# Optimization experiments

Hardware: AMD Instinct MI355X
Metric: run time of the kernel (lower is better)

The kernel has to match this reference:

```python
import jax, jax.numpy as jnp
import numpy as np
import math

B, S, F, H, E = 2, 1024, 512, 2048, 8
EPS = 1e-10

def setup_inputs() -> dict:
    key = jax.random.key(0)
    ks = jax.random.split(key, 6)
    s1 = math.sqrt(1.0 / (F + H))  # complex_xavier_init std for F->H
    s2 = math.sqrt(1.0 / (H + F))  # std for H->F
    return {
        'x_r': jax.random.normal(ks[0], (B, S, F), jnp.float32),
        'x_i': jax.random.normal(ks[1], (B, S, F), jnp.float32),
        'Wr1': jax.random.normal(ks[2], (E, F, H), jnp.float32) * s1,
        'Wi1': jax.random.normal(ks[3], (E, F, H), jnp.float32) * s1,
        'br1': jnp.zeros((E, H), jnp.float32),
        'bi1': jnp.zeros((E, H), jnp.float32),
        'mb': jnp.zeros((E, H), jnp.float32),  # ModReLU bias
        'Wr2': jax.random.normal(ks[4], (E, H, F), jnp.float32) * s2,
        'Wi2': jax.random.normal(ks[5], (E, H, F), jnp.float32) * s2,
        'br2': jnp.zeros((E, F), jnp.float32),
        'bi2': jnp.zeros((E, F), jnp.float32),
    }

def reference(x_r, x_i, Wr1, Wi1, br1, bi1, mb, Wr2, Wi2, br2, bi2):
    n_exp = Wr1.shape[0]
    # --- PhaseRouter: deterministic top-1 routing by mean token phase ---
    phase = jnp.arctan2(x_i, x_r)                      # angle(x), (B,S,F)
    mean_cos = jnp.mean(jnp.cos(phase), axis=-1)
    mean_sin = jnp.mean(jnp.sin(phase), axis=-1)
    token_phase = jnp.arctan2(mean_sin, mean_cos)      # (B,S)
    norm_phase = (token_phase + jnp.pi) / (2 * jnp.pi)
    idx = jnp.clip(jnp.floor(norm_phase * n_exp).astype(jnp.int32), 0, n_exp - 1)
    probs = jax.nn.one_hot(idx, n_exp, dtype=x_r.dtype)  # (B,S,E)
    # --- dense all-expert complex MLP (as in source: every expert on every token) ---
    # layer 1: complex linear F->H, per expert
    h_r = (jnp.einsum('bsf,efh->ebsh', x_r, Wr1) - jnp.einsum('bsf,efh->ebsh', x_i, Wi1)
           + br1[:, None, None, :])
    h_i = (jnp.einsum('bsf,efh->ebsh', x_r, Wi1) + jnp.einsum('bsf,efh->ebsh', x_i, Wr1)
           + bi1[:, None, None, :])
    # ModReLU: relu(|z|+b) * z/(|z|+eps)
    amp = jnp.sqrt(h_r * h_r + h_i * h_i + EPS)
    scale = jax.nn.relu(amp + mb[:, None, None, :]) / (amp + EPS)
    h_r = scale * h_r
    h_i = scale * h_i
    # layer 2: complex linear H->F, per expert
    y_r = (jnp.einsum('ebsh,ehf->ebsf', h_r, Wr2) - jnp.einsum('ebsh,ehf->ebsf', h_i, Wi2)
           + br2[:, None, None, :])
    y_i = (jnp.einsum('ebsh,ehf->ebsf', h_r, Wi2) + jnp.einsum('ebsh,ehf->ebsf', h_i, Wr2)
           + bi2[:, None, None, :])
    # combine: expert_weight * mask == probs * probs (one-hot, 0/1)
    w = probs * probs                                   # (B,S,E)
    out_r = jnp.einsum('ebsf,bse->bsf', y_r, w)
    out_i = jnp.einsum('ebsf,bse->bsf', y_i, w)
    return jnp.stack([out_r, out_i])                    # (2,B,S,F): real, imag
```

## Files before the change

kernel.cpp:

```cpp
#include <hip/hip_runtime.h>
#include <hip/hip_bf16.h>

#define TOKENS 2048
#define FDIM 512
#define HDIM 2048
#define NEXP 8
#define PI_F 3.14159265358979323846f

typedef __attribute__((ext_vector_type(8))) short bf16x8;
typedef __attribute__((ext_vector_type(4))) float f32x4;

__device__ __forceinline__ unsigned short f2bf(float f) {
  unsigned int u = __float_as_uint(f);
  unsigned int r = (u + 0x7fffu + ((u >> 16) & 1u)) >> 16;
  return (unsigned short)r;
}

__device__ __forceinline__ void gload16(const void* g, void* l) {
  __builtin_amdgcn_global_load_lds(
      (const __attribute__((address_space(1))) unsigned int*)g,
      (__attribute__((address_space(3))) unsigned int*)l, 16, 0, 0);
}

template<int K, int N>
__device__ __forceinline__ void pack_w_body64(
    const float* __restrict__ Wr, const float* __restrict__ Wi,
    short* __restrict__ Wp, int b, float (*tr)[33], float (*ti)[33])
{
  constexpr int NT_ = N / 32;
  int per_e = (K / 64) * NT_;
  int e = b / per_e;
  int rem = b % per_e;
  int k0 = (rem / NT_) * 64, n0 = (rem % NT_) * 32;
  int tid = threadIdx.x;
  int row = tid >> 2, c8 = (tid & 3) * 8;
  const float* wr = Wr + ((size_t)e * K + k0 + row) * N + n0 + c8;
  const float* wi = Wi + ((size_t)e * K + k0 + row) * N + n0 + c8;
  float4 a0 = *(const float4*)(wr);
  float4 a1 = *(const float4*)(wr + 4);
  float4 b0 = *(const float4*)(wi);
  float4 b1 = *(const float4*)(wi + 4);
  *(float4*)&tr[row][c8] = a0;  *(float4*)&tr[row][c8 + 4] = a1;
  *(float4*)&ti[row][c8] = b0;  *(float4*)&ti[row][c8 + 4] = b1;
  __syncthreads();
  int nl = tid >> 3, k8 = (tid & 7) * 8;
  unsigned short pr[8], pi[8];
  #pragma unroll
  for (int j = 0; j < 8; ++j) {
    pr[j] = f2bf(tr[k8 + j][nl]);
    pi[j] = f2bf(ti[k8 + j][nl]);
  }
  size_t d0 = (((size_t)e * 2 + 0) * N + n0 + nl) * K + k0 + k8;
  size_t d1 = (((size_t)e * 2 + 1) * N + n0 + nl) * K + k0 + k8;
  *(int4*)(Wp + d0) = *(const int4*)pr;
  *(int4*)(Wp + d1) = *(const int4*)pi;
}

template<int K, int N>
__device__ __forceinline__ void pack_w2x(
    const float* __restrict__ Wr, const float* __restrict__ Wi,
    short* __restrict__ Wp, int b, float (*tr)[33], float (*ti)[33])
{
  constexpr int NT_ = N / 32;
  int per_e = (K / 128) * NT_;
  int e = b / per_e;
  int rem = b % per_e;
  int k0 = (rem / NT_) * 128, n0 = (rem % NT_) * 32;
  int tid = threadIdx.x;
  int row = tid >> 2, c8 = (tid & 3) * 8;
  const float* wr = Wr + ((size_t)e * K + k0 + row) * N + n0 + c8;
  const float* wi = Wi + ((size_t)e * K + k0 + row) * N + n0 + c8;
  const float* wr1 = wr + (size_t)64 * N;
  const float* wi1 = wi + (size_t)64 * N;
  float4 a00 = *(const float4*)(wr);
  float4 a01 = *(const float4*)(wr + 4);
  float4 b00 = *(const float4*)(wi);
  float4 b01 = *(const float4*)(wi + 4);
  float4 a10 = *(const float4*)(wr1);
  float4 a11 = *(const float4*)(wr1 + 4);
  float4 b10 = *(const float4*)(wi1);
  float4 b11 = *(const float4*)(wi1 + 4);
  int nl = tid >> 3, k8 = (tid & 7) * 8;
  size_t d0 = (((size_t)e * 2 + 0) * N + n0 + nl) * K + k0 + k8;
  size_t d1 = (((size_t)e * 2 + 1) * N + n0 + nl) * K + k0 + k8;
  *(float4*)&tr[row][c8] = a00;  *(float4*)&tr[row][c8 + 4] = a01;
  *(float4*)&ti[row][c8] = b00;  *(float4*)&ti[row][c8 + 4] = b01;
  __syncthreads();
  {
    unsigned short pr[8], pi[8];
    #pragma unroll
    for (int j = 0; j < 8; ++j) {
      pr[j] = f2bf(tr[k8 + j][nl]);
      pi[j] = f2bf(ti[k8 + j][nl]);
    }
    *(int4*)(Wp + d0) = *(const int4*)pr;
    *(int4*)(Wp + d1) = *(const int4*)pi;
  }
  __syncthreads();
  *(float4*)&tr[row][c8] = a10;  *(float4*)&tr[row][c8 + 4] = a11;
  *(float4*)&ti[row][c8] = b10;  *(float4*)&ti[row][c8 + 4] = b11;
  __syncthreads();
  {
    unsigned short pr[8], pi[8];
    #pragma unroll
    for (int j = 0; j < 8; ++j) {
      pr[j] = f2bf(tr[k8 + j][nl]);
      pi[j] = f2bf(ti[k8 + j][nl]);
    }
    *(int4*)(Wp + d0 + 64) = *(const int4*)pr;
    *(int4*)(Wp + d1 + 64) = *(const int4*)pi;
  }
}

__global__ __launch_bounds__(256, 2) void route_packx_w1_kernel(
    const float* __restrict__ xr, const float* __restrict__ xi,
    int* __restrict__ idx,
    short* __restrict__ Ar, short* __restrict__ Ai,
    const float* __restrict__ Wr1, const float* __restrict__ Wi1,
    short* __restrict__ W1p)
{
  __shared__ float tr[64][33], ti[64][33];
  int bid = blockIdx.x;
  if (bid < 256) {
    int tid = threadIdx.x;
    int t = bid * 8 + (tid >> 5);
    int l = tid & 31;
    const float* r  = xr + (size_t)t * FDIM;
    const float* im = xi + (size_t)t * FDIM;
    float sc = 0.f, ss = 0.f;
    #pragma unroll
    for (int p = 0; p < 4; ++p) {
      int f = p * 128 + l * 4;
      float4 a4 = *(const float4*)(r + f);
      float4 b4 = *(const float4*)(im + f);
      float av[4] = {a4.x, a4.y, a4.z, a4.w};
      float bv[4] = {b4.x, b4.y, b4.z, b4.w};
      #pragma unroll
      for (int j = 0; j < 4; ++j) {
        float h2 = av[j] * av[j] + bv[j] * bv[j];
        if (h2 > 0.f) {
          float rs = rsqrtf(h2);
          sc += av[j] * rs;
          ss += bv[j] * rs;
        } else {
          sc += 1.f;
        }
      }
    }
    #pragma unroll
    for (int off = 16; off > 0; off >>= 1) {
      sc += __shfl_down(sc, off, 32);
      ss += __shfl_down(ss, off, 32);
    }
    if (l == 0) {
      float phase = atan2f(ss, sc);
      float norm = (phase + PI_F) / (2.f * PI_F);
      int e = (int)floorf(norm * (float)NEXP);
      e = min(max(e, 0), NEXP - 1);
      idx[t] = e;
    }
  } else if (bid < 256 + 1024) {
    int gid = (bid - 256) * 256 + threadIdx.x;
    int i = gid >> 7;
    int c4 = (gid & 127) * 4;
    float4 r = *(const float4*)(xr + (size_t)i * FDIM + c4);
    float4 m = *(const float4*)(xi + (size_t)i * FDIM + c4);
    unsigned short orr[4] = { f2bf(r.x), f2bf(r.y), f2bf(r.z), f2bf(r.w) };
    unsigned short oii[4] = { f2bf(m.x), f2bf(m.y), f2bf(m.z), f2bf(m.w) };
    *(int2*)(Ar + (size_t)i * FDIM + c4) = *(const int2*)orr;
    *(int2*)(Ai + (size_t)i * FDIM + c4) = *(const int2*)oii;
  } else {
    pack_w2x<FDIM, HDIM>(Wr1, Wi1, W1p, bid - 1280, tr, ti);
  }
}

__global__ __launch_bounds__(256) void scatter_kernel(
    const int* __restrict__ idx, int* __restrict__ counts,
    int* __restrict__ offs, int* __restrict__ perm, int* __restrict__ rexp)
{
  __shared__ int base_e[NEXP];
  __shared__ int totals[NEXP];
  __shared__ int tcnt[256][NEXP];
  int tid = threadIdx.x;
  int t0 = tid * 8;
  int eo[8];
  int loc[NEXP];
  #pragma unroll
  for (int e = 0; e < NEXP; ++e) loc[e] = 0;
  #pragma unroll
  for (int j = 0; j < 8; ++j) { eo[j] = idx[t0 + j]; loc[eo[j]]++; }
  #pragma unroll
  for (int e = 0; e < NEXP; ++e) tcnt[tid][e] = loc[e];
  __syncthreads();
  if (tid < NEXP) {
    int e = tid, run = 0;
    for (int i = 0; i < 256; ++i) { int v = tcnt[i][e]; tcnt[i][e] = run; run += v; }
    totals[e] = run;
    counts[e] = run;
  }
  __syncthreads();
  if (tid == 0) {
    int acc = 0;
    for (int e = 0; e < NEXP; ++e) { base_e[e] = acc; offs[e] = acc; acc += totals[e]; }
  }
  __syncthreads();
  #pragma unroll
  for (int e = 0; e < NEXP; ++e) loc[e] = base_e[e] + tcnt[tid][e];
  #pragma unroll
  for (int j = 0; j < 8; ++j) {
    int e = eo[j];
    int pos = loc[e]++;
    perm[pos] = t0 + j;
    rexp[pos] = e;
  }
}

template<int LDK, int NC, int NX, int NSPLIT, bool IS_L1>
__device__ __forceinline__ void gemm_body(
    int gbid, int xcd, short* AsB, short* WsB,
    const short* __restrict__ Apr, const short* __restrict__ Api,
    const short* __restrict__ Wp,
    const int* __restrict__ counts, const int* __restrict__ offs,
    const int* __restrict__ perm,
    const float* __restrict__ bre, const float* __restrict__ bim,
    const float* __restrict__ mb,
    short* __restrict__ Or, short* __restrict__ Oi,
    unsigned int* __restrict__ P)
{
  constexpr int PBE = NX * 8 * NSPLIT;
  constexpr int KCH = LDK / NSPLIT;
  constexpr int KT = KCH / 32;
  int virt = xcd * PBE + (gbid >> 3);
  int e = virt / PBE, rem = virt % PBE;
  int x = rem % NX;
  int q = rem / NX;
  int y = q & 7, s = q >> 3;
  int cnt = counts[e];
  int row0 = y * 64;
  if (row0 >= cnt) return;
  int base = offs[e];
  int n0c = x * 64;
  int kbase = s * KCH;

  int tid = threadIdx.x;
  int lane = tid & 63;
  int w = tid >> 6, wm = w >> 1, wn = w & 1;
  int lr = lane & 15, g = lane >> 4;
  int ssw = g ^ ((lr >> 1) & 3);

  int srl = tid >> 2, slt = tid & 3;
  int sc = (slt ^ ((srl >> 1) & 3)) * 16;
  int arow = min(row0 + srl, cnt - 1);
  size_t asrc;
  if constexpr (IS_L1) asrc = (size_t)perm[base + arow] * LDK + kbase;
  else                 asrc = (size_t)(base + arow) * LDK + kbase;
  const char* pAr = (const char*)(Apr + asrc) + sc;
  const char* pAi = (const char*)(Api + asrc) + sc;
  const short* We = Wp + (size_t)e * 2 * NC * LDK;
  const char* pW0 = (const char*)(We + (size_t)(n0c + srl) * LDK + kbase) + sc;
  const char* pW1 = (const char*)(We + ((size_t)NC + n0c + srl) * LDK + kbase) + sc;

  auto STAGE = [&](int buf, int t) {
    char* ab = (char*)AsB + buf * 8192;
    gload16(pAr + t * 64, ab + tid * 16);
    gload16(pAi + t * 64, ab + 4096 + tid * 16);
    char* wb = (char*)WsB + buf * 8192;
    gload16(pW0 + t * 64, wb + tid * 16);
    gload16(pW1 + t * 64, wb + 4096 + tid * 16);
  };

  f32x4 accr[2][2], acci[2][2];
  #pragma unroll
  for (int m = 0; m < 2; ++m)
    #pragma unroll
    for (int n = 0; n < 2; ++n) { accr[m][n] = 0.f; acci[m][n] = 0.f; }

  const bf16x8 SGN = {(short)0x8000, (short)0x8000, (short)0x8000, (short)0x8000,
                      (short)0x8000, (short)0x8000, (short)0x8000, (short)0x8000};

  auto COMPUTE = [&](int buf) {
    const short* Ab = AsB + buf * 4096;
    const short* Wb = WsB + buf * 4096;
    bf16x8 ar[2], ai[2], wr[2], wi[2], wni[2];
    #pragma unroll
    for (int m = 0; m < 2; ++m) {
      int off = (wm * 32 + m * 16 + lr) * 32 + ssw * 8;
      ar[m] = *(const bf16x8*)(Ab + off);
      ai[m] = *(const bf16x8*)(Ab + 2048 + off);
    }
    #pragma unroll
    for (int n = 0; n < 2; ++n) {
      int offw = (wn * 32 + n * 16 + lr) * 32 + ssw * 8;
      wr[n] = *(const bf16x8*)(Wb + offw);
      wi[n] = *(const bf16x8*)(Wb + 2048 + offw);
      wni[n] = wi[n] ^ SGN;
    }
    #pragma unroll
    for (int m = 0; m < 2; ++m)
      #pragma unroll
      for (int n = 0; n < 2; ++n) {
        accr[m][n] = __builtin_amdgcn_mfma_f32_16x16x32_bf16(ar[m], wr[n],  accr[m][n], 0, 0, 0);
        accr[m][n] = __builtin_amdgcn_mfma_f32_16x16x32_bf16(ai[m], wni[n], accr[m][n], 0, 0, 0);
        acci[m][n] = __builtin_amdgcn_mfma_f32_16x16x32_bf16(ar[m], wi[n],  acci[m][n], 0, 0, 0);
        acci[m][n] = __builtin_amdgcn_mfma_f32_16x16x32_bf16(ai[m], wr[n],  acci[m][n], 0, 0, 0);
      }
  };

  STAGE(0, 0);
  int cur = 0;
  for (int t = 0; t < KT; ++t) {
    __syncthreads();
    if (t + 1 < KT) STAGE(cur ^ 1, t + 1);
    COMPUTE(cur);
    cur ^= 1;
  }

  #pragma unroll
  for (int m = 0; m < 2; ++m) {
    #pragma unroll
    for (int qq = 0; qq < 4; ++qq) {
      int row = row0 + wm * 32 + m * 16 + g * 4 + qq;
      if (row >= cnt) continue;
      #pragma unroll
      for (int n = 0; n < 2; ++n) {
        int c = n0c + wn * 32 + n * 16 + lr;
        if constexpr (IS_L1) {
          float hr = accr[m][n][qq] + bre[e * NC + c];
          float hi = acci[m][n][qq] + bim[e * NC + c];
          float s2 = hr * hr + hi * hi + 1e-10f;
          float rr = __frsqrt_rn(s2);
          float amp = s2 * rr;
          float scl = fmaxf(amp + mb[e * NC + c], 0.f) * rr;
          Or[(size_t)(base + row) * NC + c] = (short)f2bf(hr * scl);
          Oi[(size_t)(base + row) * NC + c] = (short)f2bf(hi * scl);
        } else {
          unsigned pv = (unsigned)f2bf(accr[m][n][qq])
                      | ((unsigned)f2bf(acci[m][n][qq]) << 16);
          P[((size_t)s * TOKENS + base + row) * 512 + c] = pv;
        }
      }
    }
  }
}

__global__ __launch_bounds__(256) void gemm1_packw2_kernel(
    const short* __restrict__ A1r, const short* __restrict__ A1i,
    const short* __restrict__ W1p,
    const int* __restrict__ counts, const int* __restrict__ offs,
    const int* __restrict__ perm,
    const float* __restrict__ br1, const float* __restrict__ bi1,
    const float* __restrict__ mb,
    short* __restrict__ A2r, short* __restrict__ A2i,
    const float* __restrict__ Wr2, const float* __restrict__ Wi2,
    short* __restrict__ W2p)
{
  __shared__ __align__(16) short As[2][2][64][32];
  __shared__ __align__(16) short Ws[2][2][64][32];
  int bid = blockIdx.x;
  int r3 = bid % 3;
  if (r3 == 0) {
    int g = bid / 3;
    gemm_body<FDIM, HDIM, 32, 1, true>(g, bid & 7, &As[0][0][0][0], &Ws[0][0][0][0],
        A1r, A1i, W1p, counts, offs, perm, br1, bi1, mb, A2r, A2i, nullptr);
  } else {
    int pb = (bid / 3) * 2 + (r3 - 1);
    float (*tr)[33] = (float (*)[33])&As[0][0][0][0];
    float (*ti)[33] = (float (*)[33])&Ws[0][0][0][0];
    pack_w_body64<HDIM, FDIM>(Wr2, Wi2, W2p, pb, tr, ti);
  }
}

__global__ __launch_bounds__(256) void gemm2_kernel(
    const short* __restrict__ A2r, const short* __restrict__ A2i,
    const short* __restrict__ W2p,
    const int* __restrict__ counts, const int* __restrict__ offs,
    unsigned int* __restrict__ P)
{
  __shared__ __align__(16) short As[2][2][64][32];
  __shared__ __align__(16) short Ws[2][2][64][32];
  int bid = blockIdx.x;
  gemm_body<HDIM, FDIM, 8, 4, false>(bid, bid & 7, &As[0][0][0][0], &Ws[0][0][0][0],
      A2r, A2i, W2p, counts, offs, nullptr, nullptr, nullptr, nullptr,
      nullptr, nullptr, P);
}

__global__ __launch_bounds__(256) void finalize_kernel(
    const unsigned int* __restrict__ P, const float* __restrict__ br2,
    const float* __restrict__ bi2, const int* __restrict__ perm,
    const int* __restrict__ rexp, float* __restrict__ out)
{
  int gid = blockIdx.x * 256 + threadIdx.x;
  int i = gid >> 7;
  int c4 = (gid & 127) * 4;
  float sr[4] = {0.f, 0.f, 0.f, 0.f}, si[4] = {0.f, 0.f, 0.f, 0.f};
  #pragma unroll
  for (int s = 0; s < 4; ++s) {
    uint4 u = *(const uint4*)(P + ((size_t)s * TOKENS + i) * 512 + c4);
    unsigned uv[4] = {u.x, u.y, u.z, u.w};
    #pragma unroll
    for (int j = 0; j < 4; ++j) {
      sr[j] += __uint_as_float(uv[j] << 16);
      si[j] += __uint_as_float(uv[j] & 0xFFFF0000u);
    }
  }
  int e = rexp[i], tok = perm[i];
  float4 br = *(const float4*)(br2 + e * FDIM + c4);
  float4 bi = *(const float4*)(bi2 + e * FDIM + c4);
  float4 vr = {sr[0] + br.x, sr[1] + br.y, sr[2] + br.z, sr[3] + br.w};
  float4 vi = {si[0] + bi.x, si[1] + bi.y, si[2] + bi.z, si[3] + bi.w};
  *(float4*)(out + (size_t)tok * FDIM + c4) = vr;
  *(float4*)(out + (size_t)TOKENS * FDIM + (size_t)tok * FDIM + c4) = vi;
}

extern "C" void kernel_launch(void* const* d_in, const int* in_sizes, int n_in,
                              void* d_out, int out_size, void* d_ws, size_t ws_size,
                              hipStream_t stream)
{
  const float* xr  = (const float*)d_in[0];
  const float* xi  = (const float*)d_in[1];
  const float* Wr1 = (const float*)d_in[2];
  const float* Wi1 = (const float*)d_in[3];
  const float* br1 = (const float*)d_in[4];
  const float* bi1 = (const float*)d_in[5];
  const float* mb  = (const float*)d_in[6];
  const float* Wr2 = (const float*)d_in[7];
  const float* Wi2 = (const float*)d_in[8];
  const float* br2 = (const float*)d_in[9];
  const float* bi2 = (const float*)d_in[10];
  float* out = (float*)d_out;

  char* ws = (char*)d_ws;
  int* counts = (int*)(ws + 0);
  int* offs   = (int*)(ws + 64);
  int* idx    = (int*)(ws + 128);
  int* perm   = (int*)(ws + 8320);
  int* rexp   = (int*)(ws + 16512);

  size_t off = 32768;
  short* A1r = (short*)(ws + off); off += (size_t)TOKENS * FDIM * 2;
  short* A1i = (short*)(ws + off); off += (size_t)TOKENS * FDIM * 2;
  short* A2r = (short*)(ws + off); off += (size_t)TOKENS * HDIM * 2;
  short* A2i = (short*)(ws + off); off += (size_t)TOKENS * HDIM * 2;
  short* W1p = (short*)(ws + off); off += (size_t)NEXP * 2 * HDIM * FDIM * 2;
  short* W2p = (short*)(ws + off); off += (size_t)NEXP * 2 * FDIM * HDIM * 2;
  unsigned int* P = (unsigned int*)(ws + off);

  route_packx_w1_kernel<<<256 + 1024 + 2048, 256, 0, stream>>>(
      xr, xi, idx, A1r, A1i, Wr1, Wi1, W1p);
  scatter_kernel<<<1, 256, 0, stream>>>(idx, counts, offs, perm, rexp);

  gemm1_packw2_kernel<<<6144, 256, 0, stream>>>(
      A1r, A1i, W1p, counts, offs, perm, br1, bi1, mb, A2r, A2i, Wr2, Wi2, W2p);
  gemm2_kernel<<<2048, 256, 0, stream>>>(A2r, A2i, W2p, counts, offs, P);

  finalize_kernel<<<TOKENS * 128 / 256, 256, 0, stream>>>(
      P, br2, bi2, perm, rexp, out);
}
```

Baseline: 111.3 us.

## Move W2 packing from gemm1 kernel into first prep kernel

New measurement: 117.5 us. +5.6%, slower.

```diff
diff --git a/kernel.cpp b/kernel.cpp
--- a/kernel.cpp
+++ b/kernel.cpp
@@ -20,40 +20,6 @@
   __builtin_amdgcn_global_load_lds(
       (const __attribute__((address_space(1))) unsigned int*)g,
       (__attribute__((address_space(3))) unsigned int*)l, 16, 0, 0);
-}
-
-template<int K, int N>
-__device__ __forceinline__ void pack_w_body64(
-    const float* __restrict__ Wr, const float* __restrict__ Wi,
-    short* __restrict__ Wp, int b, float (*tr)[33], float (*ti)[33])
-{
-  constexpr int NT_ = N / 32;
-  int per_e = (K / 64) * NT_;
-  int e = b / per_e;
-  int rem = b % per_e;
-  int k0 = (rem / NT_) * 64, n0 = (rem % NT_) * 32;
-  int tid = threadIdx.x;
-  int row = tid >> 2, c8 = (tid & 3) * 8;
-  const float* wr = Wr + ((size_t)e * K + k0 + row) * N + n0 + c8;
-  const float* wi = Wi + ((size_t)e * K + k0 + row) * N + n0 + c8;
-  float4 a0 = *(const float4*)(wr);
-  float4 a1 = *(const float4*)(wr + 4);
-  float4 b0 = *(const float4*)(wi);
-  float4 b1 = *(const float4*)(wi + 4);
-  *(float4*)&tr[row][c8] = a0;  *(float4*)&tr[row][c8 + 4] = a1;
-  *(float4*)&ti[row][c8] = b0;  *(float4*)&ti[row][c8 + 4] = b1;
-  __syncthreads();
-  int nl = tid >> 3, k8 = (tid & 7) * 8;
-  unsigned short pr[8], pi[8];
-  #pragma unroll
-  for (int j = 0; j < 8; ++j) {
-    pr[j] = f2bf(tr[k8 + j][nl]);
-    pi[j] = f2bf(ti[k8 + j][nl]);
-  }
-  size_t d0 = (((size_t)e * 2 + 0) * N + n0 + nl) * K + k0 + k8;
-  size_t d1 = (((size_t)e * 2 + 1) * N + n0 + nl) * K + k0 + k8;
-  *(int4*)(Wp + d0) = *(const int4*)pr;
-  *(int4*)(Wp + d1) = *(const int4*)pi;
 }
 
 template<int K, int N>
@@ -112,12 +78,14 @@
   }
 }
 
-__global__ __launch_bounds__(256, 2) void route_packx_w1_kernel(
+__global__ __launch_bounds__(256, 2) void route_packx_w_kernel(
     const float* __restrict__ xr, const float* __restrict__ xi,
     int* __restrict__ idx,
     short* __restrict__ Ar, short* __restrict__ Ai,
     const float* __restrict__ Wr1, const float* __restrict__ Wi1,
-    short* __restrict__ W1p)
+    short* __restrict__ W1p,
+    const float* __restrict__ Wr2, const float* __restrict__ Wi2,
+    short* __restrict__ W2p)
 {
   __shared__ float tr[64][33], ti[64][33];
   int bid = blockIdx.x;
@@ -169,8 +137,10 @@
     unsigned short oii[4] = { f2bf(m.x), f2bf(m.y), f2bf(m.z), f2bf(m.w) };
     *(int2*)(Ar + (size_t)i * FDIM + c4) = *(const int2*)orr;
     *(int2*)(Ai + (size_t)i * FDIM + c4) = *(const int2*)oii;
+  } else if (bid < 256 + 1024 + 2048) {
+    pack_w2x<FDIM, HDIM>(Wr1, Wi1, W1p, bid - 1280, tr, ti);
   } else {
-    pack_w2x<FDIM, HDIM>(Wr1, Wi1, W1p, bid - 1280, tr, ti);
+    pack_w2x<HDIM, FDIM>(Wr2, Wi2, W2p, bid - 3328, tr, ti);
   }
 }
 
@@ -343,31 +313,20 @@
   }
 }
 
-__global__ __launch_bounds__(256) void gemm1_packw2_kernel(
+__global__ __launch_bounds__(256) void gemm1_kernel(
     const short* __restrict__ A1r, const short* __restrict__ A1i,
     const short* __restrict__ W1p,
     const int* __restrict__ counts, const int* __restrict__ offs,
     const int* __restrict__ perm,
     const float* __restrict__ br1, const float* __restrict__ bi1,
     const float* __restrict__ mb,
-    short* __restrict__ A2r, short* __restrict__ A2i,
-    const float* __restrict__ Wr2, const float* __restrict__ Wi2,
-    short* __restrict__ W2p)
+    short* __restrict__ A2r, short* __restrict__ A2i)
 {
   __shared__ __align__(16) short As[2][2][64][32];
   __shared__ __align__(16) short Ws[2][2][64][32];
   int bid = blockIdx.x;
-  int r3 = bid % 3;
-  if (r3 == 0) {
-    int g = bid / 3;
-    gemm_body<FDIM, HDIM, 32, 1, true>(g, bid & 7, &As[0][0][0][0], &Ws[0][0][0][0],
-        A1r, A1i, W1p, counts, offs, perm, br1, bi1, mb, A2r, A2i, nullptr);
-  } else {
-    int pb = (bid / 3) * 2 + (r3 - 1);
-    float (*tr)[33] = (float (*)[33])&As[0][0][0][0];
-    float (*ti)[33] = (float (*)[33])&Ws[0][0][0][0];
-    pack_w_body64<HDIM, FDIM>(Wr2, Wi2, W2p, pb, tr, ti);
-  }
+  gemm_body<FDIM, HDIM, 32, 1, true>(bid, bid & 7, &As[0][0][0][0], &Ws[0][0][0][0],
+      A1r, A1i, W1p, counts, offs, perm, br1, bi1, mb, A2r, A2i, nullptr);
 }
 
 __global__ __launch_bounds__(256) void gemm2_kernel(
@@ -445,12 +404,12 @@
   short* W2p = (short*)(ws + off); off += (size_t)NEXP * 2 * FDIM * HDIM * 2;
   unsigned int* P = (unsigned int*)(ws + off);
 
-  route_packx_w1_kernel<<<256 + 1024 + 2048, 256, 0, stream>>>(
-      xr, xi, idx, A1r, A1i, Wr1, Wi1, W1p);
+  route_packx_w_kernel<<<256 + 1024 + 2048 + 2048, 256, 0, stream>>>(
+      xr, xi, idx, A1r, A1i, Wr1, Wi1, W1p, Wr2, Wi2, W2p);
   scatter_kernel<<<1, 256, 0, stream>>>(idx, counts, offs, perm, rexp);
 
-  gemm1_packw2_kernel<<<6144, 256, 0, stream>>>(
-      A1r, A1i, W1p, counts, offs, perm, br1, bi1, mb, A2r, A2i, Wr2, Wi2, W2p);
+  gemm1_kernel<<<2048, 256, 0, stream>>>(
+      A1r, A1i, W1p, counts, offs, perm, br1, bi1, mb, A2r, A2i);
   gemm2_kernel<<<2048, 256, 0, stream>>>(A2r, A2i, W2p, counts, offs, P);
 
   finalize_kernel<<<TOKENS * 128 / 256, 256, 0, stream>>>(
```
